# Optimization experiments

Measured on AMD Instinct MI355X. Metric: run time of the kernel, lower is better.

The kernel has to match this reference:

```python
import math
import jax
import jax.numpy as jnp
import numpy as np

N_IMG = 8
A = 3
H = 100
W = 100
STRIDE = 16
IMG = 1600
PRE_NMS_TOP_N = 2000
POST_NMS_TOP_N = 1000
NMS_THRESH = 0.7
MIN_SIZE = 0
BBOX_XFORM_CLIP = math.log(1000.0 / 16.0)


def setup_inputs() -> dict:
    key = jax.random.key(0)
    k1, k2 = jax.random.split(key)
    objectness = jax.random.normal(k1, (N_IMG, A, H, W), jnp.float32)
    box_regression = jax.random.normal(k2, (N_IMG, A * 4, H, W), jnp.float32) * 0.5
    # Grid anchors, flattened in (H, W, A) order to match objectness.permute(0,2,3,1)
    cy = (jnp.arange(H, dtype=jnp.float32) + 0.5) * STRIDE  # [H]
    cx = (jnp.arange(W, dtype=jnp.float32) + 0.5) * STRIDE  # [W]
    half = jnp.array([64.0, 128.0, 256.0], jnp.float32) / 2.0  # [A]
    cy = cy[:, None, None]  # [H,1,1]
    cx = cx[None, :, None]  # [1,W,1]
    s = half[None, None, :]  # [1,1,A]
    x1, y1, x2, y2 = jnp.broadcast_arrays(cx - s, cy - s, cx + s, cy + s)
    anc = jnp.stack([x1, y1, x2, y2], axis=-1).reshape(-1, 4)  # [H*W*A, 4]
    anchors = jnp.broadcast_to(anc[None], (N_IMG, H * W * A, 4)).copy()
    return {
        "objectness": objectness,
        "box_regression": box_regression,
        "anchors": anchors,
        "image_height": IMG,
        "image_width": IMG,
    }


def _decode(deltas, boxes):
    # BoxCoder(weights=(1,1,1,1)).decode with TO_REMOVE=1
    widths = boxes[..., 2] - boxes[..., 0] + 1.0
    heights = boxes[..., 3] - boxes[..., 1] + 1.0
    ctr_x = boxes[..., 0] + 0.5 * widths
    ctr_y = boxes[..., 1] + 0.5 * heights
    dx, dy = deltas[..., 0], deltas[..., 1]
    dw = jnp.minimum(deltas[..., 2], BBOX_XFORM_CLIP)
    dh = jnp.minimum(deltas[..., 3], BBOX_XFORM_CLIP)
    pcx = dx * widths + ctr_x
    pcy = dy * heights + ctr_y
    pw = jnp.exp(dw) * widths
    ph = jnp.exp(dh) * heights
    return jnp.stack(
        [pcx - 0.5 * pw, pcy - 0.5 * ph, pcx + 0.5 * pw - 1.0, pcy + 0.5 * ph - 1.0],
        axis=-1,
    )


def _nms_keep(boxes, valid, thresh):
    # boxes [n,4] sorted by descending score; valid: pre-filter mask.
    n = boxes.shape[0]
    x1, y1, x2, y2 = boxes[:, 0], boxes[:, 1], boxes[:, 2], boxes[:, 3]
    areas = (x2 - x1 + 1.0) * (y2 - y1 + 1.0)
    xx1 = jnp.maximum(x1[:, None], x1[None, :])
    yy1 = jnp.maximum(y1[:, None], y1[None, :])
    xx2 = jnp.minimum(x2[:, None], x2[None, :])
    yy2 = jnp.minimum(y2[:, None], y2[None, :])
    inter = jnp.maximum(xx2 - xx1 + 1.0, 0.0) * jnp.maximum(yy2 - yy1 + 1.0, 0.0)
    iou = inter / (areas[:, None] + areas[None, :] - inter)
    idx = jnp.arange(n)

    def body(i, keep):
        sup = keep[i] & (iou[i] > thresh) & (idx > i)
        return keep & ~sup

    return jax.lax.fori_loop(0, n, body, valid)


def _forward(objectness, box_regression, anchors, image_height, image_width):
    N, A_, H_, W_ = objectness.shape
    scores = jax.nn.sigmoid(objectness.transpose(0, 2, 3, 1).reshape(N, -1))  # [N, A*H*W]
    deltas = (
        box_regression.reshape(N, A_, 4, H_, W_)
        .transpose(0, 3, 4, 1, 2)
        .reshape(N, -1, 4)
    )
    pre = min(PRE_NMS_TOP_N, scores.shape[1])
    top_scores, top_idx = jax.lax.top_k(scores, pre)  # sorted descending
    deltas = jnp.take_along_axis(deltas, top_idx[:, :, None], axis=1)
    anc = jnp.take_along_axis(anchors, top_idx[:, :, None], axis=1)
    props = _decode(deltas, anc)  # [N, pre, 4]
    # clip to image (fact = 1)
    xs = jnp.clip(props[..., 0::2], 0.0, image_width - 1.0)
    ys = jnp.clip(props[..., 1::2], 0.0, image_height - 1.0)
    props = jnp.stack([xs[..., 0], ys[..., 0], xs[..., 1], ys[..., 1]], axis=-1)
    # filter small / out-of-image-center boxes
    ws = props[..., 2] - props[..., 0] + 1.0
    hs = props[..., 3] - props[..., 1] + 1.0
    xc = props[..., 0] + ws / 2.0
    yc = props[..., 1] + hs / 2.0
    valid = (ws >= MIN_SIZE) & (hs >= MIN_SIZE) & (xc < image_width) & (yc < image_height)
    keep = jax.vmap(lambda b, v: _nms_keep(b, v, NMS_THRESH))(props, valid)

    def _select(b, s, k):
        # compact kept boxes (already score-sorted) into fixed-size output
        rank = jnp.cumsum(k) - 1
        tgt = jnp.where(k & (rank < POST_NMS_TOP_N), rank, POST_NMS_TOP_N)
        ob = jnp.zeros((POST_NMS_TOP_N + 1, 4), b.dtype).at[tgt].set(b)[:POST_NMS_TOP_N]
        os = jnp.zeros((POST_NMS_TOP_N + 1,), s.dtype).at[tgt].set(s)[:POST_NMS_TOP_N]
        ov = jnp.arange(POST_NMS_TOP_N) < jnp.minimum(jnp.sum(k), POST_NMS_TOP_N)
        return ob, os, ov

    return jax.vmap(_select)(props, top_scores, keep)


def reference(objectness, box_regression, anchors, image_height, image_width):
    # Returns (boxes [N,post,4], objectness scores [N,post], valid mask [N,post])
    return _forward(objectness, box_regression, anchors, image_height, image_width)
```

## Files before the change

### kernel.cpp

```cpp
#include <hip/hip_runtime.h>
#include <math.h>
#include <stdint.h>

#define NIMG   8
#define NA     30000
#define NQ4    7500
#define PRE_N  2000
#define POST_N 1000
#define NMS_TH 0.7f
#define DCLIP  4.135166556742356f
#define IMGF   1600.0f
#define IMGM1  1599.0f
#define CAND_MAX 4096
#define HPITCH 4104
#define BIG_BIN 64
#define PREF_BIN 3064u


__device__ __forceinline__ void decode_store(
    uint64_t key, unsigned int rank, int n, const float* __restrict__ breg,
    float* __restrict__ wsBoxes, float* __restrict__ wsScores,
    int* __restrict__ wsValid)
{
    unsigned int idx = (unsigned int)key;
    unsigned int k   = ~((unsigned int)(key >> 32));
    unsigned int u   = (k & 0x80000000u) ? (k & 0x7fffffffu) : ~k;
    float logit = __uint_as_float(u);
    float score = 1.0f / (1.0f + expf(-logit));

    int a = idx % 3, t = idx / 3, w = t % 100, h = t / 100;
    const float* bp = breg + n*120000 + (a*4)*10000 + t;
    float dx = bp[0], dy = bp[10000], dw = bp[20000], dh = bp[30000];

    float half = (a == 0) ? 32.0f : ((a == 1) ? 64.0f : 128.0f);
    float cx = w * 16.0f + 8.0f, cy = h * 16.0f + 8.0f;
    float x1 = cx - half, y1 = cy - half, x2 = cx + half, y2 = cy + half;
    float wd = x2 - x1 + 1.0f, hg = y2 - y1 + 1.0f;
    float cxr = x1 + 0.5f * wd, cyr = y1 + 0.5f * hg;
    dw = fminf(dw, DCLIP); dh = fminf(dh, DCLIP);
    float pcx = dx * wd + cxr, pcy = dy * hg + cyr;
    float pw = expf(dw) * wd, ph = expf(dh) * hg;
    float px1 = pcx - 0.5f * pw, py1 = pcy - 0.5f * ph;
    float px2 = pcx + 0.5f * pw - 1.0f, py2 = pcy + 0.5f * ph - 1.0f;
    px1 = fminf(fmaxf(px1, 0.0f), IMGM1);
    px2 = fminf(fmaxf(px2, 0.0f), IMGM1);
    py1 = fminf(fmaxf(py1, 0.0f), IMGM1);
    py2 = fminf(fmaxf(py2, 0.0f), IMGM1);
    float wss = px2 - px1 + 1.0f, hss = py2 - py1 + 1.0f;
    float xc = px1 + wss * 0.5f, yc = py1 + hss * 0.5f;
    int valid = (wss >= 0.0f) && (hss >= 0.0f) && (xc < IMGF) && (yc < IMGF);

    ((float4*)wsBoxes)[n * PRE_N + (int)rank] = make_float4(px1, py1, px2, py2);
    wsScores[n * PRE_N + (int)rank] = score;
    wsValid [n * PRE_N + (int)rank] = valid;
}

__device__ __forceinline__ unsigned int keyof(float f) {
    unsigned int u = __float_as_uint(f);
    return (u & 0x80000000u) ? ~u : (u | 0x80000000u);
}

__global__ __launch_bounds__(1024) void topk_decode(
    const float* __restrict__ obj, const float* __restrict__ breg,
    float* __restrict__ wsBoxes, float* __restrict__ wsScores,
    int* __restrict__ wsValid)
{
    const int n    = blockIdx.x;
    const int tid  = threadIdx.x;
    const int lane = tid & 63;
    const int wid  = tid >> 6;
    const int rep  = wid & 3;

    __shared__ unsigned int   histf[4 * HPITCH];
    __shared__ unsigned short sufx[4096];
    __shared__ uint64_t       grp[CAND_MAX];
    __shared__ uint64_t       grp2[CAND_MAX];
    __shared__ unsigned int   wsum[16];
    __shared__ unsigned int   sbstar;
    __shared__ unsigned int   lbbase[16];
    __shared__ unsigned int   lbcnt, lbtot;

    unsigned int*   hist2  = histf;
    unsigned short* sufx2  = (unsigned short*)(histf + HPITCH);
    unsigned char*  bin2lb = (unsigned char*)(histf + 2 * HPITCH);

    for (int b = tid; b < 4 * HPITCH; b += 1024) histf[b] = 0u;
    __syncthreads();

    const float4* obj4 = (const float4*)(obj + n * NA);
    float4 v[8];
    #pragma unroll
    for (int kk = 0; kk < 7; ++kk) v[kk] = obj4[tid + kk * 1024];
    v[7] = make_float4(0.f, 0.f, 0.f, 0.f);
    if (tid < NQ4 - 7 * 1024) v[7] = obj4[tid + 7 * 1024];

    #pragma unroll
    for (int kk = 0; kk < 8; ++kk) {
        if (kk == 7 && tid >= NQ4 - 7 * 1024) continue;
        const float fv[4] = {v[kk].x, v[kk].y, v[kk].z, v[kk].w};
        #pragma unroll
        for (int e = 0; e < 4; ++e) {
            unsigned int b = keyof(fv[e]) >> 20;
            if (b >= PREF_BIN)
                atomicAdd(&histf[rep * HPITCH + b], 1u);
        }
    }
    __syncthreads();

    unsigned int c0, c1, c2, c3;
    {
        const int b0 = tid * 4;
        c0 = histf[b0+0] + histf[HPITCH+b0+0] + histf[2*HPITCH+b0+0] + histf[3*HPITCH+b0+0];
        c1 = histf[b0+1] + histf[HPITCH+b0+1] + histf[2*HPITCH+b0+1] + histf[3*HPITCH+b0+1];
        c2 = histf[b0+2] + histf[HPITCH+b0+2] + histf[2*HPITCH+b0+2] + histf[3*HPITCH+b0+2];
        c3 = histf[b0+3] + histf[HPITCH+b0+3] + histf[2*HPITCH+b0+3] + histf[3*HPITCH+b0+3];
    }
    unsigned int p = c0 + c1 + c2 + c3;
    unsigned int s = p;
    #pragma unroll
    for (int off = 1; off < 64; off <<= 1) {
        unsigned int vv = __shfl_down(s, off);
        if (lane + off < 64) s += vv;
    }
    if (lane == 0) wsum[wid] = s;
    __syncthreads();
    unsigned int ftotal = 0;
    for (int w = 0; w < 16; ++w) ftotal += wsum[w];

    if (ftotal < PRE_N) {
        #pragma unroll
        for (int kk = 0; kk < 8; ++kk) {
            if (kk == 7 && tid >= NQ4 - 7 * 1024) continue;
            const float fv[4] = {v[kk].x, v[kk].y, v[kk].z, v[kk].w};
            #pragma unroll
            for (int e = 0; e < 4; ++e) {
                unsigned int b = keyof(fv[e]) >> 20;
                if (b < PREF_BIN)
                    atomicAdd(&histf[rep * HPITCH + b], 1u);
            }
        }
        __syncthreads();
        {
            const int b0 = tid * 4;
            c0 = histf[b0+0] + histf[HPITCH+b0+0] + histf[2*HPITCH+b0+0] + histf[3*HPITCH+b0+0];
            c1 = histf[b0+1] + histf[HPITCH+b0+1] + histf[2*HPITCH+b0+1] + histf[3*HPITCH+b0+1];
            c2 = histf[b0+2] + histf[HPITCH+b0+2] + histf[2*HPITCH+b0+2] + histf[3*HPITCH+b0+2];
            c3 = histf[b0+3] + histf[HPITCH+b0+3] + histf[2*HPITCH+b0+3] + histf[3*HPITCH+b0+3];
        }
        p = c0 + c1 + c2 + c3;
        s = p;
        #pragma unroll
        for (int off = 1; off < 64; off <<= 1) {
            unsigned int vv = __shfl_down(s, off);
            if (lane + off < 64) s += vv;
        }
        __syncthreads();
        if (lane == 0) wsum[wid] = s;
        __syncthreads();
    }

    unsigned int wafter = 0;
    for (int w = wid + 1; w < 16; ++w) wafter += wsum[w];
    unsigned int after = (s - p) + wafter;
    {
        unsigned int S3 = after + c3;
        unsigned int S2 = S3 + c2;
        unsigned int S1 = S2 + c1;
        unsigned int S0 = S1 + c0;
        if (S3 >= PRE_N && after < PRE_N) { sbstar = tid*4+3; }
        if (S2 >= PRE_N && S3    < PRE_N) { sbstar = tid*4+2; }
        if (S1 >= PRE_N && S2    < PRE_N) { sbstar = tid*4+1; }
        if (S0 >= PRE_N && S1    < PRE_N) { sbstar = tid*4+0; }
        sufx[tid*4+0] = (unsigned short)S1;
        sufx[tid*4+1] = (unsigned short)S2;
        sufx[tid*4+2] = (unsigned short)S3;
        sufx[tid*4+3] = (unsigned short)after;

        const unsigned int st[4] = {S1, S2, S3, after};
        #pragma unroll
        for (int q = 0; q < 4; ++q) {
            const int b = tid*4 + q;
            unsigned int base = st[q];
            #pragma unroll
            for (int r = 0; r < 4; ++r) {
                unsigned int c = histf[r * HPITCH + b];
                histf[r * HPITCH + b] = base;
                base += c;
            }
        }
    }
    __syncthreads();
    const unsigned int bstar = sbstar;

    #pragma unroll
    for (int kk = 0; kk < 8; ++kk) {
        if (kk == 7 && tid >= NQ4 - 7 * 1024) continue;
        const float fv[4] = {v[kk].x, v[kk].y, v[kk].z, v[kk].w};
        #pragma unroll
        for (int e = 0; e < 4; ++e) {
            unsigned int k = keyof(fv[e]);
            unsigned int b = k >> 20;
            if (b < bstar) continue;
            int j = (tid + kk * 1024) * 4 + e;
            int a = j / 10000, t = j - a * 10000;
            uint64_t key = (((uint64_t)(~k)) << 32) | (unsigned int)(t * 3 + a);
            unsigned int slot = atomicAdd(&histf[rep * HPITCH + b], 1u);
            if (slot < CAND_MAX) grp[slot] = key;
        }
    }
    __syncthreads();

    const unsigned int total = min(histf[3 * HPITCH + bstar], (unsigned int)CAND_MAX);

    ((unsigned int*)bin2lb)[tid] = 0xFFFFFFFFu;
    hist2[tid] = 0u; hist2[tid+1024] = 0u; hist2[tid+2048] = 0u; hist2[tid+3072] = 0u;
    if (tid == 0) { lbcnt = 0u; lbtot = 0u; }
    __syncthreads();

    #pragma unroll
    for (int q = 0; q < 4; ++q) {
        const unsigned int b = (unsigned int)(tid*4 + q);
        if (b >= bstar) {
            const unsigned int ge  = min(histf[3*HPITCH + b], (unsigned int)CAND_MAX);
            const unsigned int cnt = ge - (unsigned int)sufx[b];
            if (cnt > (unsigned int)BIG_BIN) {
                unsigned int pos = atomicAdd(&lbcnt, 1u);
                if (pos < 16u) {
                    bin2lb[b] = (unsigned char)pos;
                    lbbase[pos] = atomicAdd(&lbtot, cnt);
                }
            }
        }
    }
    __syncthreads();

    for (unsigned int slot = tid; slot < total; slot += 1024) {
        const unsigned int hi = (unsigned int)(grp[slot] >> 32);
        const unsigned int b  = 4095u - (hi >> 20);
        const unsigned char lb = bin2lb[b];
        if (lb != 0xFFu)
            atomicAdd(&hist2[(unsigned int)lb * 256u + ((hi >> 12) & 0xFFu)], 1u);
    }
    __syncthreads();

    {
        const unsigned int nlb = min(lbcnt, 16u);
        if ((unsigned int)wid < nlb) {
            const int xb = wid * 256 + lane * 4;
            unsigned int e0 = hist2[xb+0], e1 = hist2[xb+1],
                         e2 = hist2[xb+2], e3 = hist2[xb+3];
            unsigned int tsum = e0 + e1 + e2 + e3;
            unsigned int inc = tsum;
            #pragma unroll
            for (int off = 1; off < 64; off <<= 1) {
                unsigned int vv = __shfl_up(inc, off);
                if (lane >= off) inc += vv;
            }
            unsigned int base = lbbase[wid] + (inc - tsum);
            hist2[xb+0] = base;             sufx2[xb+0] = (unsigned short)base;
            base += e0; hist2[xb+1] = base; sufx2[xb+1] = (unsigned short)base;
            base += e1; hist2[xb+2] = base; sufx2[xb+2] = (unsigned short)base;
            base += e2; hist2[xb+3] = base; sufx2[xb+3] = (unsigned short)base;
        }
    }
    __syncthreads();

    for (unsigned int slot = tid; slot < total; slot += 1024) {
        const uint64_t key = grp[slot];
        const unsigned int hi = (unsigned int)(key >> 32);
        const unsigned int b  = 4095u - (hi >> 20);
        const unsigned char lb = bin2lb[b];
        if (lb != 0xFFu) {
            unsigned int d = atomicAdd(&hist2[(unsigned int)lb * 256u + ((hi >> 12) & 0xFFu)], 1u);
            grp2[d] = key;
        }
    }
    __syncthreads();

    for (unsigned int slot = tid; slot < total; slot += 1024) {
        const uint64_t key = grp[slot];
        const unsigned int hi = (unsigned int)(key >> 32);
        const unsigned int b  = 4095u - (hi >> 20);
        const unsigned int gbeg = sufx[b];
        const unsigned int gend = min(histf[3 * HPITCH + b], (unsigned int)CAND_MAX);
        const unsigned char lb  = bin2lb[b];
        unsigned int rank;

        if (lb != 0xFFu) {
            const unsigned int x   = (unsigned int)lb * 256u + ((hi >> 12) & 0xFFu);
            const unsigned int s2  = sufx2[x];
            const unsigned int e2v = hist2[x];
            rank = gbeg + (s2 - lbbase[lb]);
            for (unsigned int g = s2; g < e2v; g += 8u) {
                #pragma unroll
                for (int i = 0; i < 8; ++i) {
                    const unsigned int gi = g + (unsigned int)i;
                    const uint64_t vv = grp2[min(gi, e2v - 1u)];
                    rank += (gi < e2v && vv < key) ? 1u : 0u;
                }
            }
        } else {
            rank = gbeg;
            unsigned int g = gbeg;
            for (; g + 8u <= gend; g += 8u) {
                uint64_t v0 = grp[g+0], v1 = grp[g+1], v2 = grp[g+2], v3 = grp[g+3];
                uint64_t v4 = grp[g+4], v5 = grp[g+5], v6 = grp[g+6], v7 = grp[g+7];
                unsigned int r0 = (v0 < key) ? 1u : 0u;
                r0 += (v1 < key) ? 1u : 0u;
                r0 += (v2 < key) ? 1u : 0u;
                r0 += (v3 < key) ? 1u : 0u;
                r0 += (v4 < key) ? 1u : 0u;
                r0 += (v5 < key) ? 1u : 0u;
                r0 += (v6 < key) ? 1u : 0u;
                r0 += (v7 < key) ? 1u : 0u;
                rank += r0;
            }
            for (; g < gend; ++g)
                rank += (grp[g] < key) ? 1u : 0u;
        }
        if (rank >= PRE_N) continue;
        decode_store(key, rank, n, breg, wsBoxes, wsScores, wsValid);
    }
}

__global__ __launch_bounds__(512) void nms_mask(
    const float* __restrict__ wsBoxes, uint64_t* __restrict__ mask)
{
    const int blk  = blockIdx.x;
    const int n    = blk >> 5;
    const int i_t  = blk & 31;
    const int tid  = threadIdx.x;
    const int lane = tid & 63;
    const int wv   = tid >> 6;

    __shared__ uint64_t tile[64 * 33];

    for (int idx = tid; idx < 64 * 33; idx += 512) tile[idx] = 0ull;
    __syncthreads();

    const int r = i_t * 64 + lane;
    float4 rb = (r < PRE_N) ? ((const float4*)wsBoxes)[n * PRE_N + r]
                            : make_float4(0.f, 0.f, 0.f, 0.f);
    float ra = (rb.z - rb.x + 1.0f) * (rb.w - rb.y + 1.0f);

    for (int j_t = i_t + wv; j_t < 32; j_t += 8) {
        const int j = j_t * 64 + lane;
        float4 cb = (j < PRE_N) ? ((const float4*)wsBoxes)[n * PRE_N + j]
                                : make_float4(3e30f, 3e30f, 3e30f, 3e30f);
        float ca = (cb.z - cb.x + 1.0f) * (cb.w - cb.y + 1.0f);
        const uint64_t jmask = (j_t == 31) ? 0xFFFFull : ~0ull;
        const bool diag = (j_t == i_t);
        uint64_t myword = 0ull;

        #pragma unroll
        for (int c = 0; c < 64; ++c) {
            float rx1 = __int_as_float(__builtin_amdgcn_readlane(__float_as_int(rb.x), c));
            float ry1 = __int_as_float(__builtin_amdgcn_readlane(__float_as_int(rb.y), c));
            float rx2 = __int_as_float(__builtin_amdgcn_readlane(__float_as_int(rb.z), c));
            float ry2 = __int_as_float(__builtin_amdgcn_readlane(__float_as_int(rb.w), c));
            float rar = __int_as_float(__builtin_amdgcn_readlane(__float_as_int(ra), c));
            float xx1 = fmaxf(rx1, cb.x), yy1 = fmaxf(ry1, cb.y);
            float xx2 = fminf(rx2, cb.z), yy2 = fminf(ry2, cb.w);
            float ww = fmaxf(xx2 - xx1 + 1.0f, 0.0f);
            float hh = fmaxf(yy2 - yy1 + 1.0f, 0.0f);
            float inter = ww * hh;
            float denom = rar + ca - inter;
            unsigned long long bits = __ballot(inter > NMS_TH * denom) & jmask;
            if (diag) bits &= (c == 63) ? 0ull : ((~0ull) << (c + 1));
            if (lane == c) myword = bits;
        }
        tile[lane * 33 + j_t] = myword;
    }
    __syncthreads();

    uint64_t* mrow = mask + ((size_t)n * PRE_N + (size_t)i_t * 64) * 32;
    const int cmax = (i_t == 31) ? 16 : 64;
    for (int idx = tid; idx < cmax * 32; idx += 512) {
        const int rr = idx >> 5, w = idx & 31;
        mrow[idx] = tile[rr * 33 + w];
    }
}

#define NSA(b) \
    "v_readlane_b32 %[tlo], %[cl], " #b "\n\t" \
    "v_readlane_b32 %[thi], %[ch], " #b "\n\t" \
    "s_bitcmp1_b32 %[wlo], " #b "\n\t" \
    "s_cselect_b32 %[m], 0, -1\n\t" \
    "s_and_b32 %[tlo], %[tlo], %[m]\n\t" \
    "s_and_b32 %[thi], %[thi], %[m]\n\t" \
    "s_or_b32 %[wlo], %[wlo], %[tlo]\n\t" \
    "s_or_b32 %[whi], %[whi], %[thi]\n\t"

#define NSB(b, c) \
    "v_readlane_b32 %[tlo], %[cl], " #b "\n\t" \
    "v_readlane_b32 %[thi], %[ch], " #b "\n\t" \
    "s_bitcmp1_b32 %[whi], " #c "\n\t" \
    "s_cselect_b32 %[m], 0, -1\n\t" \
    "s_and_b32 %[tlo], %[tlo], %[m]\n\t" \
    "s_and_b32 %[thi], %[thi], %[m]\n\t" \
    "s_or_b32 %[wlo], %[wlo], %[tlo]\n\t" \
    "s_or_b32 %[whi], %[whi], %[thi]\n\t"

__global__ __launch_bounds__(512) void nms_scan_select(
    const float* __restrict__ wsBoxes, const float* __restrict__ wsScores,
    const int* __restrict__ wsValid, const uint64_t* __restrict__ mask,
    float* __restrict__ out)
{
    const int n    = blockIdx.x;
    const int tid  = threadIdx.x;
    const int lane = tid & 63;
    const int wid  = tid >> 6;

    __shared__ unsigned int sup[64];
    __shared__ unsigned int kml, kmh;
    __shared__ int skept, sdone;
    __shared__ int sscan[256];

    if (tid < 64) sup[tid] = 0u;
    if (tid == 0) { skept = 0; sdone = 0; }
    __syncthreads();

    if (tid < 500) {
        int4 vv = ((const int4*)(wsValid + n * PRE_N))[tid];
        unsigned int nib = (vv.x ? 0u : 1u) | ((vv.y ? 0u : 1u) << 1)
                         | ((vv.z ? 0u : 1u) << 2) | ((vv.w ? 0u : 1u) << 3);
        if (nib) atomicOr(&sup[tid >> 3], nib << ((tid & 7) * 4));
    } else {
        atomicOr(&sup[tid >> 3], 0xFu << ((tid & 7) * 4));
    }
    __syncthreads();

    const uint64_t* mrow = mask + (size_t)n * PRE_N * 32;

    const int r0 = (tid >> 5) * 4;
    const int w  = tid & 31;
    uint64_t pfc[4], pfn[4];
    #pragma unroll
    for (int q = 0; q < 4; ++q) {
        const int r = r0 + q;
        pfn[q] = (w > 0 && r < PRE_N) ? mrow[(size_t)r * 32 + w] : 0ull;
    }

    unsigned int cl = 0u, ch = 0u;
    if (wid == 0) {
        uint64_t cw = (lane < PRE_N) ? mrow[(size_t)lane * 32 + 0] : 0ull;
        cl = (unsigned int)cw; ch = (unsigned int)(cw >> 32);
    }

    for (int g = 0; g < 32; ++g) {
        __syncthreads();
        if (sdone) break;

        #pragma unroll
        for (int q = 0; q < 4; ++q) pfc[q] = pfn[q];
        if (g < 31) {
            #pragma unroll
            for (int q = 0; q < 4; ++q) {
                const int r = (g + 1) * 64 + r0 + q;
                pfn[q] = (w > g + 1 && r < PRE_N) ? mrow[(size_t)r * 32 + w] : 0ull;
            }
        }

        if (wid == 0) {
            unsigned int nl = 0u, nh = 0u;
            if (g < 31) {
                const int r = (g + 1) * 64 + lane;
                uint64_t cw = (r < PRE_N) ? mrow[(size_t)r * 32 + (g + 1)] : 0ull;
                nl = (unsigned int)cw; nh = (unsigned int)(cw >> 32);
            }

            unsigned int wlo = (unsigned int)__builtin_amdgcn_readfirstlane((int)sup[2*g]);
            unsigned int whi = (unsigned int)__builtin_amdgcn_readfirstlane((int)sup[2*g+1]);
            int tlo_, thi_, m_;
            asm volatile(
                NSA(0)  NSA(1)  NSA(2)  NSA(3)  NSA(4)  NSA(5)  NSA(6)  NSA(7)
                NSA(8)  NSA(9)  NSA(10) NSA(11) NSA(12) NSA(13) NSA(14) NSA(15)
                NSA(16) NSA(17) NSA(18) NSA(19) NSA(20) NSA(21) NSA(22) NSA(23)
                NSA(24) NSA(25) NSA(26) NSA(27) NSA(28) NSA(29) NSA(30) NSA(31)
                NSB(32,0)  NSB(33,1)  NSB(34,2)  NSB(35,3)
                NSB(36,4)  NSB(37,5)  NSB(38,6)  NSB(39,7)
                NSB(40,8)  NSB(41,9)  NSB(42,10) NSB(43,11)
                NSB(44,12) NSB(45,13) NSB(46,14) NSB(47,15)
                NSB(48,16) NSB(49,17) NSB(50,18) NSB(51,19)
                NSB(52,20) NSB(53,21) NSB(54,22) NSB(55,23)
                NSB(56,24) NSB(57,25) NSB(58,26) NSB(59,27)
                NSB(60,28) NSB(61,29) NSB(62,30) NSB(63,31)
                : [wlo]"+s"(wlo), [whi]"+s"(whi),
                  [tlo]"=&s"(tlo_), [thi]"=&s"(thi_), [m]"=&s"(m_)
                : [cl]"v"(cl), [ch]"v"(ch)
                : "scc");

            if (lane == 0) {
                sup[2*g]     = wlo;
                sup[2*g + 1] = whi;
                unsigned int kl = ~wlo, kh = ~whi;
                kml = kl; kmh = kh;
                int nk = skept + __popc(kl) + __popc(kh);
                skept = nk;
                if (nk >= POST_N) sdone = 1;
            }
            cl = nl; ch = nh;
        }
        __syncthreads();

        if (!sdone && w > g) {
            const unsigned long long km =
                ((unsigned long long)kmh << 32) | kml;
            unsigned long long acc = 0ull;
            #pragma unroll
            for (int q = 0; q < 4; ++q) {
                if ((km >> (r0 + q)) & 1ull) acc |= pfc[q];
            }
            if (acc) {
                atomicOr(&sup[2*w],     (unsigned int)acc);
                atomicOr(&sup[2*w + 1], (unsigned int)(acc >> 32));
            }
        }
    }
    __syncthreads();

    int c[8];
    int lsum = 0;
    const int base8 = tid * 8;
    if (tid < 256) {
        for (int q = 0; q < 8; ++q) {
            const int i = base8 + q;
            c[q] = (i < PRE_N) ? (int)((~sup[i >> 5] >> (i & 31)) & 1u) : 0;
            lsum += c[q];
        }
        sscan[tid] = lsum;
    }
    __syncthreads();
    for (int off = 1; off < 256; off <<= 1) {
        int v = 0;
        if (tid < 256 && tid >= off) v = sscan[tid - off];
        __syncthreads();
        if (tid < 256) sscan[tid] += v;
        __syncthreads();
    }
    const int excl  = (tid < 256) ? (sscan[tid] - lsum) : 0;
    const int total = sscan[255];

    float* ob  = out + n * POST_N * 4;
    float* osc = out + NIMG * POST_N * 4 + n * POST_N;
    float* ovd = out + NIMG * POST_N * 5 + n * POST_N;

    for (int i = tid; i < POST_N * 4; i += 512) ob[i] = 0.0f;
    for (int i = tid; i < POST_N; i += 512) osc[i] = 0.0f;
    const int lim = min(total, POST_N);
    for (int i = tid; i < POST_N; i += 512) ovd[i] = (i < lim) ? 1.0f : 0.0f;
    __syncthreads();

    if (tid < 256) {
        int run = excl;
        for (int q = 0; q < 8; ++q) {
            const int i = base8 + q;
            if (i < PRE_N && c[q]) {
                if (run < POST_N) {
                    float4 b = ((const float4*)wsBoxes)[n * PRE_N + i];
                    ob[run * 4 + 0] = b.x;
                    ob[run * 4 + 1] = b.y;
                    ob[run * 4 + 2] = b.z;
                    ob[run * 4 + 3] = b.w;
                    osc[run] = wsScores[n * PRE_N + i];
                }
                run++;
            }
        }
    }
}

extern "C" void kernel_launch(void* const* d_in, const int* in_sizes, int n_in,
                              void* d_out, int out_size, void* d_ws, size_t ws_size,
                              hipStream_t stream) {
    const float* obj  = (const float*)d_in[0];
    const float* breg = (const float*)d_in[1];
    float* ws        = (float*)d_ws;
    float* wsBoxes   = ws;
    float* wsScores  = ws + 64000;
    int*   wsValid   = (int*)(ws + 80000);
    uint64_t* wsMask = (uint64_t*)(ws + 96000);

    topk_decode<<<NIMG, 1024, 0, stream>>>(obj, breg, wsBoxes, wsScores, wsValid);
    nms_mask<<<NIMG * 32, 512, 0, stream>>>(wsBoxes, wsMask);
    nms_scan_select<<<NIMG, 512, 0, stream>>>(wsBoxes, wsScores, wsValid, wsMask,
                                              (float*)d_out);
}
```

Before: 151.5 us.

## Add multi-block prefilter kernel compacting top candidates before per-image topk

Adds a filter_compact kernel that uses 64 blocks to scan objectness and compact logits above a prefix bin into a per-image global candidate buffer. topk_decode then builds its histogram and scatter from those few thousand candidates instead of all 30000 scores, and falls back to a full scan when the count is out of range. The aim is to spread the memory-bound scan across many CUs instead of 8 blocks. In exchange it adds a memset, an extra kernel launch, global atomics, and reuse of the mask workspace as the candidate buffer.

```diff
diff --git a/kernel.cpp b/kernel.cpp
--- a/kernel.cpp
+++ b/kernel.cpp
@@ -15,6 +15,7 @@
 #define HPITCH 4104
 #define BIG_BIN 64
 #define PREF_BIN 3064u
+#define CAP    6144
 
 
 __device__ __forceinline__ void decode_store(
@@ -60,8 +61,51 @@
     return (u & 0x80000000u) ? ~u : (u | 0x80000000u);
 }
 
+__global__ __launch_bounds__(256) void filter_compact(
+    const float* __restrict__ obj,
+    uint64_t* __restrict__ candBuf, unsigned int* __restrict__ candCnt)
+{
+    const int n   = blockIdx.x >> 3;
+    const int sub = blockIdx.x & 7;
+    const int tid = threadIdx.x;
+
+    __shared__ uint64_t stage[4096];
+    __shared__ unsigned int scnt, sbase;
+    if (tid == 0) scnt = 0u;
+    __syncthreads();
+
+    const float4* obj4 = (const float4*)(obj + n * NA);
+    const int start = sub * 940;
+    const int end   = min(start + 940, NQ4);
+
+    for (int i = start + tid; i < end; i += 256) {
+        float4 fv = obj4[i];
+        const float f[4] = {fv.x, fv.y, fv.z, fv.w};
+        #pragma unroll
+        for (int e = 0; e < 4; ++e) {
+            unsigned int k = keyof(f[e]);
+            if ((k >> 20) >= PREF_BIN) {
+                int j = i * 4 + e;
+                int a = j / 10000, t = j - a * 10000;
+                uint64_t key = (((uint64_t)(~k)) << 32) | (unsigned int)(t * 3 + a);
+                unsigned int pos = atomicAdd(&scnt, 1u);
+                stage[pos] = key;
+            }
+        }
+    }
+    __syncthreads();
+    if (tid == 0) sbase = atomicAdd(&candCnt[n], scnt);
+    __syncthreads();
+    const unsigned int base = sbase, cnt = scnt;
+    for (unsigned int i = tid; i < cnt; i += 256) {
+        const unsigned int d = base + i;
+        if (d < (unsigned int)CAP) candBuf[(size_t)n * CAP + d] = stage[i];
+    }
+}
+
 __global__ __launch_bounds__(1024) void topk_decode(
     const float* __restrict__ obj, const float* __restrict__ breg,
+    const uint64_t* __restrict__ candBuf, const unsigned int* __restrict__ candCnt,
     float* __restrict__ wsBoxes, float* __restrict__ wsScores,
     int* __restrict__ wsValid)
 {
@@ -87,57 +131,16 @@
     for (int b = tid; b < 4 * HPITCH; b += 1024) histf[b] = 0u;
     __syncthreads();
 
-    const float4* obj4 = (const float4*)(obj + n * NA);
-    float4 v[8];
-    #pragma unroll
-    for (int kk = 0; kk < 7; ++kk) v[kk] = obj4[tid + kk * 1024];
-    v[7] = make_float4(0.f, 0.f, 0.f, 0.f);
-    if (tid < NQ4 - 7 * 1024) v[7] = obj4[tid + 7 * 1024];
-
-    #pragma unroll
-    for (int kk = 0; kk < 8; ++kk) {
-        if (kk == 7 && tid >= NQ4 - 7 * 1024) continue;
-        const float fv[4] = {v[kk].x, v[kk].y, v[kk].z, v[kk].w};
-        #pragma unroll
-        for (int e = 0; e < 4; ++e) {
-            unsigned int b = keyof(fv[e]) >> 20;
-            if (b >= PREF_BIN)
-                atomicAdd(&histf[rep * HPITCH + b], 1u);
-        }
-    }
-    __syncthreads();
-
-    unsigned int c0, c1, c2, c3;
-    {
-        const int b0 = tid * 4;
-        c0 = histf[b0+0] + histf[HPITCH+b0+0] + histf[2*HPITCH+b0+0] + histf[3*HPITCH+b0+0];
-        c1 = histf[b0+1] + histf[HPITCH+b0+1] + histf[2*HPITCH+b0+1] + histf[3*HPITCH+b0+1];
-        c2 = histf[b0+2] + histf[HPITCH+b0+2] + histf[2*HPITCH+b0+2] + histf[3*HPITCH+b0+2];
-        c3 = histf[b0+3] + histf[HPITCH+b0+3] + histf[2*HPITCH+b0+3] + histf[3*HPITCH+b0+3];
-    }
-    unsigned int p = c0 + c1 + c2 + c3;
-    unsigned int s = p;
-    #pragma unroll
-    for (int off = 1; off < 64; off <<= 1) {
-        unsigned int vv = __shfl_down(s, off);
-        if (lane + off < 64) s += vv;
-    }
-    if (lane == 0) wsum[wid] = s;
-    __syncthreads();
-    unsigned int ftotal = 0;
-    for (int w = 0; w < 16; ++w) ftotal += wsum[w];
-
-    if (ftotal < PRE_N) {
-        #pragma unroll
-        for (int kk = 0; kk < 8; ++kk) {
-            if (kk == 7 && tid >= NQ4 - 7 * 1024) continue;
-            const float fv[4] = {v[kk].x, v[kk].y, v[kk].z, v[kk].w};
-            #pragma unroll
-            for (int e = 0; e < 4; ++e) {
-                unsigned int b = keyof(fv[e]) >> 20;
-                if (b < PREF_BIN)
-                    atomicAdd(&histf[rep * HPITCH + b], 1u);
-            }
+    const unsigned int cc = candCnt[n];
+    const bool fast = (cc >= PRE_N) && (cc <= (unsigned int)CAP);
+    const uint64_t* cb = candBuf + (size_t)n * CAP;
+
+    unsigned int c0, c1, c2, c3, p, s;
+
+    if (fast) {
+        for (unsigned int i = tid; i < cc; i += 1024) {
+            const unsigned int hi = (unsigned int)(cb[i] >> 32);
+            atomicAdd(&histf[rep * HPITCH + (4095u - (hi >> 20))], 1u);
         }
         __syncthreads();
         {
@@ -147,18 +150,34 @@
             c2 = histf[b0+2] + histf[HPITCH+b0+2] + histf[2*HPITCH+b0+2] + histf[3*HPITCH+b0+2];
             c3 = histf[b0+3] + histf[HPITCH+b0+3] + histf[2*HPITCH+b0+3] + histf[3*HPITCH+b0+3];
         }
-        p = c0 + c1 + c2 + c3;
-        s = p;
-        #pragma unroll
-        for (int off = 1; off < 64; off <<= 1) {
-            unsigned int vv = __shfl_down(s, off);
-            if (lane + off < 64) s += vv;
+    } else {
+        const float4* obj4 = (const float4*)(obj + n * NA);
+        for (int i = tid; i < NQ4; i += 1024) {
+            float4 fv = obj4[i];
+            atomicAdd(&histf[rep * HPITCH + (keyof(fv.x) >> 20)], 1u);
+            atomicAdd(&histf[rep * HPITCH + (keyof(fv.y) >> 20)], 1u);
+            atomicAdd(&histf[rep * HPITCH + (keyof(fv.z) >> 20)], 1u);
+            atomicAdd(&histf[rep * HPITCH + (keyof(fv.w) >> 20)], 1u);
         }
         __syncthreads();
-        if (lane == 0) wsum[wid] = s;
-        __syncthreads();
-    }
-
+        {
+            const int b0 = tid * 4;
+            c0 = histf[b0+0] + histf[HPITCH+b0+0] + histf[2*HPITCH+b0+0] + histf[3*HPITCH+b0+0];
+            c1 = histf[b0+1] + histf[HPITCH+b0+1] + histf[2*HPITCH+b0+1] + histf[3*HPITCH+b0+1];
+            c2 = histf[b0+2] + histf[HPITCH+b0+2] + histf[2*HPITCH+b0+2] + histf[3*HPITCH+b0+2];
+            c3 = histf[b0+3] + histf[HPITCH+b0+3] + histf[2*HPITCH+b0+3] + histf[3*HPITCH+b0+3];
+        }
+    }
+
+    p = c0 + c1 + c2 + c3;
+    s = p;
+    #pragma unroll
+    for (int off = 1; off < 64; off <<= 1) {
+        unsigned int vv = __shfl_down(s, off);
+        if (lane + off < 64) s += vv;
+    }
+    if (lane == 0) wsum[wid] = s;
+    __syncthreads();
     unsigned int wafter = 0;
     for (int w = wid + 1; w < 16; ++w) wafter += wsum[w];
     unsigned int after = (s - p) + wafter;
@@ -192,20 +211,31 @@
     __syncthreads();
     const unsigned int bstar = sbstar;
 
-    #pragma unroll
-    for (int kk = 0; kk < 8; ++kk) {
-        if (kk == 7 && tid >= NQ4 - 7 * 1024) continue;
-        const float fv[4] = {v[kk].x, v[kk].y, v[kk].z, v[kk].w};
-        #pragma unroll
-        for (int e = 0; e < 4; ++e) {
-            unsigned int k = keyof(fv[e]);
-            unsigned int b = k >> 20;
+    if (fast) {
+        for (unsigned int i = tid; i < cc; i += 1024) {
+            const uint64_t key = cb[i];
+            const unsigned int hi = (unsigned int)(key >> 32);
+            const unsigned int b  = 4095u - (hi >> 20);
             if (b < bstar) continue;
-            int j = (tid + kk * 1024) * 4 + e;
-            int a = j / 10000, t = j - a * 10000;
-            uint64_t key = (((uint64_t)(~k)) << 32) | (unsigned int)(t * 3 + a);
             unsigned int slot = atomicAdd(&histf[rep * HPITCH + b], 1u);
             if (slot < CAND_MAX) grp[slot] = key;
+        }
+    } else {
+        const float4* obj4 = (const float4*)(obj + n * NA);
+        for (int i = tid; i < NQ4; i += 1024) {
+            float4 fv = obj4[i];
+            const float f[4] = {fv.x, fv.y, fv.z, fv.w};
+            #pragma unroll
+            for (int e = 0; e < 4; ++e) {
+                unsigned int k = keyof(f[e]);
+                unsigned int b = k >> 20;
+                if (b < bstar) continue;
+                int j = i * 4 + e;
+                int a = j / 10000, t = j - a * 10000;
+                uint64_t key = (((uint64_t)(~k)) << 32) | (unsigned int)(t * 3 + a);
+                unsigned int slot = atomicAdd(&histf[rep * HPITCH + b], 1u);
+                if (slot < CAND_MAX) grp[slot] = key;
+            }
         }
     }
     __syncthreads();
@@ -580,8 +610,13 @@
     float* wsScores  = ws + 64000;
     int*   wsValid   = (int*)(ws + 80000);
     uint64_t* wsMask = (uint64_t*)(ws + 96000);
-
-    topk_decode<<<NIMG, 1024, 0, stream>>>(obj, breg, wsBoxes, wsScores, wsValid);
+    uint64_t*     candBuf = wsMask;
+    unsigned int* candCnt = (unsigned int*)(wsMask + (size_t)NIMG * CAP);
+
+    hipMemsetAsync(candCnt, 0, NIMG * sizeof(unsigned int), stream);
+    filter_compact<<<NIMG * 8, 256, 0, stream>>>(obj, candBuf, candCnt);
+    topk_decode<<<NIMG, 1024, 0, stream>>>(obj, breg, candBuf, candCnt,
+                                           wsBoxes, wsScores, wsValid);
     nms_mask<<<NIMG * 32, 512, 0, stream>>>(wsBoxes, wsMask);
     nms_scan_select<<<NIMG, 512, 0, stream>>>(wsBoxes, wsScores, wsValid, wsMask,
                                               (float*)d_out);
```

New measurement: 157.0 us. +3.7%, slower.
